# Performance work log

Hardware: AMD Instinct MI355X
Metric: run time of the kernel (lower is better)

## Reference

```python
import jax, jax.numpy as jnp
import numpy as np

NUM_HEADS = 16
THETA = 10000.0


def _rope(x, cos, sin):
    # x: [B, H, S, d_k]; cos/sin: [S, d_k//2]
    x_even = x[..., 0::2]
    x_odd = x[..., 1::2]
    out_even = x_even * cos - x_odd * sin
    out_odd = x_odd * cos + x_even * sin
    # interleave back to original even/odd layout
    return jnp.stack([out_even, out_odd], axis=-1).reshape(x.shape)


def setup_inputs() -> dict:
    key = jax.random.key(0)
    ks = jax.random.split(key, 5)
    B, S, D = 2, 2048, 1024
    std = 2.0 / (D + D)
    return {
        "x": jax.random.normal(ks[0], (B, S, D), dtype=jnp.float32),
        "w_q": jax.random.normal(ks[1], (D, D), dtype=jnp.float32) * std,
        "w_k": jax.random.normal(ks[2], (D, D), dtype=jnp.float32) * std,
        "w_v": jax.random.normal(ks[3], (D, D), dtype=jnp.float32) * std,
        "w_o": jax.random.normal(ks[4], (D, D), dtype=jnp.float32) * std,
    }


def reference(x, w_q, w_k, w_v, w_o):
    B, S, D = x.shape
    H = NUM_HEADS
    d_k = D // H

    # QKV projections: x @ W.T
    q = jnp.einsum('bsd,ed->bse', x, w_q).reshape(B, S, H, d_k).transpose(0, 2, 1, 3)
    k = jnp.einsum('bsd,ed->bse', x, w_k).reshape(B, S, H, d_k).transpose(0, 2, 1, 3)
    v = jnp.einsum('bsd,ed->bse', x, w_v).reshape(B, S, H, d_k).transpose(0, 2, 1, 3)

    # RoPE (token_positions = arange(S))
    pos = jnp.arange(S, dtype=jnp.float32)
    inv_freq = 1.0 / (THETA ** (2.0 * jnp.arange(d_k // 2, dtype=jnp.float32) / d_k))
    angles = pos[:, None] * inv_freq[None, :]  # [S, d_k//2]
    cos, sin = jnp.cos(angles), jnp.sin(angles)
    q = _rope(q, cos, sin)
    k = _rope(k, cos, sin)

    # causal attention
    scores = jnp.einsum('bhqd,bhkd->bhqk', q, k) / jnp.sqrt(jnp.float32(d_k))
    causal = jnp.tril(jnp.ones((S, S), dtype=bool))
    scores = jnp.where(causal[None, None], scores, -jnp.inf)
    attn = jax.nn.softmax(scores, axis=-1)
    out = jnp.einsum('bhqk,bhkd->bhqd', attn, v)  # [B, H, S, d_k]

    out = out.transpose(0, 2, 1, 3).reshape(B, S, D)
    return jnp.einsum('bsd,ed->bse', out, w_o)
```

## Files before the change

kernel.cpp:

```cpp
#include <hip/hip_runtime.h>

typedef unsigned short u16;
typedef unsigned int u32;
typedef short bf16x8 __attribute__((ext_vector_type(8)));
typedef float f32x4 __attribute__((ext_vector_type(4)));

#define CSC 0.18033688011112042f

__device__ __forceinline__ u16 f2bf(float f) {
    union { float f; unsigned u; } x; x.f = f;
    unsigned r = x.u + 0x7fffu + ((x.u >> 16) & 1u);
    return (u16)(r >> 16);
}
__device__ __forceinline__ float bf2f(u16 v) {
    union { unsigned u; float f; } x; x.u = ((unsigned)v) << 16;
    return x.f;
}
__device__ __forceinline__ float exp2_fast(float x) {
#if __has_builtin(__builtin_amdgcn_exp2f)
    return __builtin_amdgcn_exp2f(x);
#else
    return exp2f(x);
#endif
}
__device__ __forceinline__ void gl_lds16(const u16* g, u16* l) {
#if __has_builtin(__builtin_amdgcn_global_load_lds)
    __builtin_amdgcn_global_load_lds(
        (const __attribute__((address_space(1))) unsigned int*)g,
        (__attribute__((address_space(3))) unsigned int*)l, 16, 0, 0);
#else
    *(bf16x8*)l = *(const bf16x8*)g;
#endif
}
__device__ __forceinline__ int ileave(int x) {
    return (x < 16) ? (x << 1) : (((x - 16) << 1) | 1);
}

__global__ void cvt_all_kernel(const float* __restrict__ x, const float* __restrict__ wq,
                               const float* __restrict__ wk, const float* __restrict__ wv,
                               const float* __restrict__ wo,
                               u16* __restrict__ xb, u16* __restrict__ qkvw,
                               u16* __restrict__ ow) {
    int i = blockIdx.x * 256 + threadIdx.x;
    const float4* src;
    ushort4* dst;
    if (i < 1048576) {
        src = (const float4*)x + i;
        dst = (ushort4*)xb + i;
    } else {
        int r = i - 1048576;
        int m = r >> 18;
        int off = r & 262143;
        const float* s4 = (m == 0) ? wq : (m == 1) ? wk : (m == 2) ? wv : wo;
        u16* d = (m < 3) ? (qkvw + (size_t)m * 1048576) : ow;
        src = (const float4*)s4 + off;
        dst = (ushort4*)d + off;
    }
    float4 v = *src;
    ushort4 o;
    o.x = f2bf(v.x); o.y = f2bf(v.y); o.z = f2bf(v.z); o.w = f2bf(v.w);
    *dst = o;
}

__global__ void rope_kernel(u16* __restrict__ qb, u16* __restrict__ kb) {
    int idx = blockIdx.x * 256 + threadIdx.x;
    u16* buf;
    float scale;
    if (blockIdx.y == 0) { buf = qb; scale = CSC; } else { buf = kb; scale = 1.0f; }
    int g   = idx & 7;
    int row = idx >> 3;
    int s   = row & 2047;
    u16* p = buf + (size_t)row * 64 + g * 8;
    bf16x8 v = *(bf16x8*)p;
    bf16x8 o;
    #pragma unroll
    for (int q = 0; q < 4; ++q) {
        int i = g * 4 + q;
        float inv = exp2_fast((float)i * -0.4152410118609203f);
        float ang = (float)s * inv;
        float sn, cs;
        sincosf(ang, &sn, &cs);
        float e  = bf2f(((u16*)&v)[2 * q]);
        float od = bf2f(((u16*)&v)[2 * q + 1]);
        ((u16*)&o)[2 * q]     = f2bf((e * cs - od * sn) * scale);
        ((u16*)&o)[2 * q + 1] = f2bf((od * cs + e * sn) * scale);
    }
    *(bf16x8*)p = o;
}

__global__ __launch_bounds__(256) void gemm_qkv(const u16* __restrict__ A,
                                                const u16* __restrict__ Bw,
                                                u16* __restrict__ C, int K) {
    __shared__ __align__(16) u16 SH[8448];
    u16* As = SH;
    u16* Bs = SH + 4096;
    const int tid  = threadIdx.x;
    const int bm   = blockIdx.x * 128;
    const int bn   = blockIdx.y * 128;
    const int wave = tid >> 6, lane = tid & 63;
    const int wm   = (wave >> 1) * 64, wn = (wave & 1) * 64;
    const int l16  = lane & 15, quad = lane >> 4;
    const int mat  = bn >> 10;

    f32x4 acc[4][4];
    #pragma unroll
    for (int i = 0; i < 4; i++)
        #pragma unroll
        for (int j = 0; j < 4; j++)
            #pragma unroll
            for (int e = 0; e < 4; e++) acc[i][j][e] = 0.0f;

    const int srow = tid >> 2, scol = (tid & 3) * 8;
    const u16* gA0 = A  + (size_t)(bm + srow) * K + scol;
    const u16* gA1 = A  + (size_t)(bm + 64 + srow) * K + scol;
    const u16* gB0 = Bw + (size_t)(bn + srow) * K + scol;
    const u16* gB1 = Bw + (size_t)(bn + 64 + srow) * K + scol;
    u16* lA0 = &As[(size_t)tid * 8];
    u16* lA1 = &As[(size_t)(tid + 256) * 8];
    u16* lB0 = &Bs[(size_t)tid * 8];
    u16* lB1 = &Bs[(size_t)(tid + 256) * 8];

    for (int k0 = 0; k0 < K; k0 += 32) {
        __syncthreads();
        gl_lds16(gA0 + k0, lA0);
        gl_lds16(gA1 + k0, lA1);
        gl_lds16(gB0 + k0, lB0);
        gl_lds16(gB1 + k0, lB1);
        __syncthreads();
        bf16x8 af[4], bfr[4];
        #pragma unroll
        for (int i = 0; i < 4; i++) af[i]  = *(const bf16x8*)&As[(wm + i * 16 + l16) * 32 + quad * 8];
        #pragma unroll
        for (int j = 0; j < 4; j++) bfr[j] = *(const bf16x8*)&Bs[(wn + j * 16 + l16) * 32 + quad * 8];
        #pragma unroll
        for (int i = 0; i < 4; i++)
            #pragma unroll
            for (int j = 0; j < 4; j++)
                acc[i][j] = __builtin_amdgcn_mfma_f32_16x16x32_bf16(af[i], bfr[j], acc[i][j], 0, 0, 0);
    }

    const int b  = bm >> 11, sb = bm & 2047;
    if (mat < 2) {
        #pragma unroll
        for (int pass = 0; pass < 2; ++pass) {
            __syncthreads();
            if ((wn >> 6) == pass) {
                #pragma unroll
                for (int i = 0; i < 4; i++)
                    #pragma unroll
                    for (int j = 0; j < 4; j++)
                        #pragma unroll
                        for (int r = 0; r < 4; r++) {
                            int rl = wm + i * 16 + quad * 4 + r;
                            int cl = j * 16 + l16;
                            SH[rl * 66 + cl] = f2bf(acc[i][j][r]);
                        }
            }
            __syncthreads();
            int rl   = tid >> 1;
            int half = (tid & 1) * 32;
            int c    = (bn + pass * 64) & 1023;
            int h    = c >> 6;
            int s    = sb + rl;
            u16* dst = C + (size_t)mat * 4194304 +
                       (((size_t)(b * 16 + h) * 2048 + s) * 64) + half;
            const u16* srcp = &SH[rl * 66 + half];
            #pragma unroll
            for (int kk = 0; kk < 4; ++kk)
                *(bf16x8*)(dst + kk * 8) = *(const bf16x8*)(srcp + kk * 8);
        }
    } else {
        #pragma unroll
        for (int pass = 0; pass < 2; ++pass) {
            __syncthreads();
            if ((wn >> 6) == pass) {
                #pragma unroll
                for (int i = 0; i < 4; i++)
                    #pragma unroll
                    for (int j = 0; j < 4; j++)
                        #pragma unroll
                        for (int r = 0; r < 4; r++) {
                            int row = j * 16 + l16;
                            int ml  = wm + i * 16 + quad * 4 + r;
                            int sp  = (ml & ~31) | ileave(ml & 31);
                            SH[row * 130 + sp] = f2bf(acc[i][j][r]);
                        }
            }
            __syncthreads();
            int row = tid >> 2, seg = tid & 3;
            int cc  = (bn + pass * 64 + row) & 1023;
            int h = cc >> 6, dv = cc & 63;
            u16* dst = C + (size_t)8388608 +
                       (((size_t)(b * 16 + h) * 64 + dv) * 2048) + sb + seg * 32;
            const u16* srcp = &SH[row * 130 + seg * 32];
            #pragma unroll
            for (int kk = 0; kk < 4; ++kk)
                *(bf16x8*)(dst + kk * 8) = *(const bf16x8*)(srcp + kk * 8);
        }
    }
}

__global__ __launch_bounds__(256, 2) void gemm_out(const u16* __restrict__ A,
                                                   const u16* __restrict__ Bw,
                                                   float* __restrict__ C, int K) {
    __shared__ __align__(16) u16 As[128 * 32];
    __shared__ __align__(16) u16 Bs[64 * 32];
    const int tid  = threadIdx.x;
    const int bm   = blockIdx.x * 128;
    const int bn   = blockIdx.y * 64;
    const int wave = tid >> 6, lane = tid & 63;
    const int wm   = wave * 32;
    const int l16  = lane & 15, quad = lane >> 4;

    f32x4 acc[2][4];
    #pragma unroll
    for (int i = 0; i < 2; i++)
        #pragma unroll
        for (int j = 0; j < 4; j++)
            #pragma unroll
            for (int e = 0; e < 4; e++) acc[i][j][e] = 0.0f;

    const int srow = tid >> 2, scol = (tid & 3) * 8;
    const u16* gA0 = A  + (size_t)(bm + srow) * K + scol;
    const u16* gA1 = A  + (size_t)(bm + 64 + srow) * K + scol;
    const u16* gB0 = Bw + (size_t)(bn + srow) * K + scol;
    u16* lA0 = &As[(size_t)tid * 8];
    u16* lA1 = &As[(size_t)(tid + 256) * 8];
    u16* lB0 = &Bs[(size_t)tid * 8];

    for (int k0 = 0; k0 < K; k0 += 32) {
        __syncthreads();
        gl_lds16(gA0 + k0, lA0);
        gl_lds16(gA1 + k0, lA1);
        gl_lds16(gB0 + k0, lB0);
        __syncthreads();
        bf16x8 af[2], bfr[4];
        #pragma unroll
        for (int i = 0; i < 2; i++) af[i]  = *(const bf16x8*)&As[(wm + i * 16 + l16) * 32 + quad * 8];
        #pragma unroll
        for (int j = 0; j < 4; j++) bfr[j] = *(const bf16x8*)&Bs[(j * 16 + l16) * 32 + quad * 8];
        #pragma unroll
        for (int i = 0; i < 2; i++)
            #pragma unroll
            for (int j = 0; j < 4; j++)
                acc[i][j] = __builtin_amdgcn_mfma_f32_16x16x32_bf16(af[i], bfr[j], acc[i][j], 0, 0, 0);
    }

    #pragma unroll
    for (int i = 0; i < 2; i++)
        #pragma unroll
        for (int j = 0; j < 4; j++)
            #pragma unroll
            for (int r = 0; r < 4; r++) {
                int mr = bm + wm + i * 16 + quad * 4 + r;
                int nc = bn + j * 16 + l16;
                C[(size_t)mr * 1024 + nc] = acc[i][j][r];
            }
}

__global__ __launch_bounds__(256, 2) void attn_kernel(const u16* __restrict__ Q,
                                                      const u16* __restrict__ Kb,
                                                      const u16* __restrict__ Vt,
                                                      u16* __restrict__ Oout) {
    __shared__ __align__(16) u16 KV[2][8192];
    __shared__ __align__(16) u16 PW[4 * 1024];
    const int tid  = threadIdx.x;
    const int wave = tid >> 6, lane = tid & 63;
    const int l16  = lane & 15, quad = lane >> 4;
    const int bid  = blockIdx.x;
    const int j    = (bid >> 3) & 15;
    const int bh   = (bid & 7) * 4 + (bid >> 7);
    const int T    = 32 - j;
    const int qA0  = j * 64 + wave * 16;
    const int qB0  = (31 - j) * 64 + wave * 16;

    const u16* Qh = Q  + (size_t)bh * 2048 * 64;
    const u16* Kh = Kb + (size_t)bh * 2048 * 64;
    const u16* Vh = Vt + (size_t)bh * 64 * 2048;

    bf16x8 qAf0 = *(const bf16x8*)&Qh[(size_t)(qA0 + l16) * 64 + quad * 8];
    bf16x8 qAf1 = *(const bf16x8*)&Qh[(size_t)(qA0 + l16) * 64 + 32 + quad * 8];
    bf16x8 qBf0 = *(const bf16x8*)&Qh[(size_t)(qB0 + l16) * 64 + quad * 8];
    bf16x8 qBf1 = *(const bf16x8*)&Qh[(size_t)(qB0 + l16) * 64 + 32 + quad * 8];

    f32x4 oA[4], oB[4];
    float lsA[4], lsB[4];
    #pragma unroll
    for (int t = 0; t < 4; t++)
        #pragma unroll
        for (int e = 0; e < 4; e++) { oA[t][e] = 0.0f; oB[t][e] = 0.0f; }
    #pragma unroll
    for (int r = 0; r < 4; r++) { lsA[r] = 0.0f; lsB[r] = 0.0f; }

    const int srow = tid >> 2;
    const int scs  = (((tid & 3) ^ ((tid >> 3) & 3))) * 8;
    const u16* gK = Kh + (size_t)srow * 64 + scs;
    const u16* gV = Vh + (size_t)srow * 2048 + scs;

    const int cswz = (quad ^ ((l16 >> 1) & 3)) * 8;
    const int psw0 = ((quad ^ (l16 & 7)) << 3);
    const int psw1 = (((quad ^ (l16 & 7)) ^ 4) << 3);

    u16* pw16 = PW + wave * 1024;
    u32* pw32 = (u32*)pw16;

    auto stage = [&](int t, int buf) {
        u16* base = KV[buf];
        gl_lds16(gK + (size_t)t * 4096,      base + (size_t)tid * 8);
        gl_lds16(gK + (size_t)t * 4096 + 32, base + 2048 + (size_t)tid * 8);
        gl_lds16(gV + (size_t)t * 64,        base + 4096 + (size_t)tid * 8);
        gl_lds16(gV + (size_t)t * 64 + 32,   base + 6144 + (size_t)tid * 8);
    };

    auto side = [&](const bf16x8& q0f, const bf16x8& q1f, bf16x8* kf0, bf16x8* kf1,
                    bf16x8* vf0, bf16x8* vf1, f32x4* o, float* ls,
                    int q0, int kbase, bool diag) {
        f32x4 s[4];
        #pragma unroll
        for (int n = 0; n < 4; n++) {
            #pragma unroll
            for (int e = 0; e < 4; e++) s[n][e] = 0.0f;
            s[n] = __builtin_amdgcn_mfma_f32_16x16x32_bf16(q0f, kf0[n], s[n], 0, 0, 0);
            s[n] = __builtin_amdgcn_mfma_f32_16x16x32_bf16(q1f, kf1[n], s[n], 0, 0, 0);
        }
        float p[4][4];
        #pragma unroll
        for (int n = 0; n < 4; n++)
            #pragma unroll
            for (int r = 0; r < 4; r++) {
                float v = exp2_fast(s[n][r]);
                if (diag) {
                    int row = q0 + quad * 4 + r;
                    v = (kbase + n * 16 + l16 > row) ? 0.0f : v;
                }
                p[n][r] = v;
                ls[r] += v;
            }
        #pragma unroll
        for (int c = 0; c < 2; c++)
            #pragma unroll
            for (int r = 0; r < 4; r++) {
                int prow = quad * 4 + r;
                int pj   = (((c * 4 + (l16 >> 2)) ^ (prow & 7)) << 2) | (l16 & 3);
                pw32[prow * 32 + pj] =
                    (u32)f2bf(p[2 * c][r]) | ((u32)f2bf(p[2 * c + 1][r]) << 16);
            }
        asm volatile("s_waitcnt lgkmcnt(0)" ::: "memory");
        bf16x8 pf0 = *(const bf16x8*)&pw16[l16 * 64 + psw0];
        bf16x8 pf1 = *(const bf16x8*)&pw16[l16 * 64 + psw1];
        #pragma unroll
        for (int dn = 0; dn < 4; dn++) {
            o[dn] = __builtin_amdgcn_mfma_f32_16x16x32_bf16(pf0, vf0[dn], o[dn], 0, 0, 0);
            o[dn] = __builtin_amdgcn_mfma_f32_16x16x32_bf16(pf1, vf1[dn], o[dn], 0, 0, 0);
        }
    };

    stage(0, 0);
    for (int t = 0; t < T; ++t) {
        __syncthreads();
        if (t + 1 < T) stage(t + 1, (t + 1) & 1);
        const u16* B = KV[t & 1];
        bf16x8 kf0[4], kf1[4], vf0[4], vf1[4];
        #pragma unroll
        for (int n = 0; n < 4; n++) {
            int ri = (n * 16 + l16) * 32 + cswz;
            kf0[n] = *(const bf16x8*)&B[ri];
            kf1[n] = *(const bf16x8*)&B[2048 + ri];
            vf0[n] = *(const bf16x8*)&B[4096 + ri];
            vf1[n] = *(const bf16x8*)&B[6144 + ri];
        }
        const int kbase = t * 64;
        side(qBf0, qBf1, kf0, kf1, vf0, vf1, oB, lsB, qB0, kbase, t == T - 1);
        if (t <= j)
            side(qAf0, qAf1, kf0, kf1, vf0, vf1, oA, lsA, qA0, kbase, t == j);
    }

    #pragma unroll
    for (int off = 1; off < 16; off <<= 1)
        #pragma unroll
        for (int r = 0; r < 4; r++) {
            lsA[r] += __shfl_xor(lsA[r], off);
            lsB[r] += __shfl_xor(lsB[r], off);
        }

    const int b = bh >> 4, h = bh & 15;
    #pragma unroll
    for (int r = 0; r < 4; r++) {
        float iA = 1.0f / lsA[r];
        float iB = 1.0f / lsB[r];
        int sA = qA0 + quad * 4 + r;
        int sB = qB0 + quad * 4 + r;
        #pragma unroll
        for (int dn = 0; dn < 4; dn++) {
            int d = h * 64 + dn * 16 + l16;
            Oout[((size_t)b * 2048 + sA) * 1024 + d] = f2bf(oA[dn][r] * iA);
            Oout[((size_t)b * 2048 + sB) * 1024 + d] = f2bf(oB[dn][r] * iB);
        }
    }
}

extern "C" void kernel_launch(void* const* d_in, const int* in_sizes, int n_in,
                              void* d_out, int out_size, void* d_ws, size_t ws_size,
                              hipStream_t stream) {
    const float* x  = (const float*)d_in[0];
    const float* wq = (const float*)d_in[1];
    const float* wk = (const float*)d_in[2];
    const float* wv = (const float*)d_in[3];
    const float* wo = (const float*)d_in[4];
    float* out = (float*)d_out;

    const int M = 4096, D = 1024;
    u16* xb    = (u16*)d_ws;
    u16* qkvw  = xb   + (size_t)M * D;
    u16* ow    = qkvw + (size_t)3 * D * D;
    u16* qkv   = ow   + (size_t)D * D;
    u16* qb    = qkv;
    u16* kb    = qkv + (size_t)M * D;
    u16* vtb   = qkv + (size_t)2 * M * D;
    u16* aob   = qkv + (size_t)3 * M * D;

    cvt_all_kernel<<<8192, 256, 0, stream>>>(x, wq, wk, wv, wo, xb, qkvw, ow);

    dim3 gq(32, 24);
    gemm_qkv<<<gq, 256, 0, stream>>>(xb, qkvw, qkv, D);

    dim3 gr(2048, 2);
    rope_kernel<<<gr, 256, 0, stream>>>(qb, kb);

    attn_kernel<<<512, 256, 0, stream>>>(qb, kb, vtb, aob);

    dim3 go(32, 16);
    gemm_out<<<go, 256, 0, stream>>>(aob, ow, out, D);
}
```

Before: 195.2 us.

## Split attention KV loop across two wave groups with LDS partial-sum merge

The attention kernel now uses 512 threads per block, with two groups of four waves each handling alternating 64-key tiles of the same query rows, so per-block KV work is split in half. Each group has its own double-buffered K/V staging region in LDS. After the loop, group 1 writes its partial O accumulators and row sums to LDS and group 0 adds them before normalising and storing. This raises wave-level parallelism for the long causal rows at the cost of doubled LDS use, an extra reduction pass, and possibly lower occupancy. The merge works by plain addition because the softmax uses a fixed scale with no running max.

Result: slower. 303.9 us (+55.7%).

```diff
diff --git a/kernel.cpp b/kernel.cpp
--- a/kernel.cpp
+++ b/kernel.cpp
@@ -258,21 +258,24 @@
             }
 }
 
-__global__ __launch_bounds__(256, 2) void attn_kernel(const u16* __restrict__ Q,
+__global__ __launch_bounds__(512, 4) void attn_kernel(const u16* __restrict__ Q,
                                                       const u16* __restrict__ Kb,
                                                       const u16* __restrict__ Vt,
                                                       u16* __restrict__ Oout) {
-    __shared__ __align__(16) u16 KV[2][8192];
-    __shared__ __align__(16) u16 PW[4 * 1024];
+    __shared__ __align__(16) u16 KV[4][8192];
+    __shared__ __align__(16) u16 PW[8 * 1024];
     const int tid  = threadIdx.x;
     const int wave = tid >> 6, lane = tid & 63;
+    const int grp  = wave >> 2;
+    const int w4   = wave & 3;
+    const int tidl = tid & 255;
     const int l16  = lane & 15, quad = lane >> 4;
     const int bid  = blockIdx.x;
     const int j    = (bid >> 3) & 15;
     const int bh   = (bid & 7) * 4 + (bid >> 7);
     const int T    = 32 - j;
-    const int qA0  = j * 64 + wave * 16;
-    const int qB0  = (31 - j) * 64 + wave * 16;
+    const int qA0  = j * 64 + w4 * 16;
+    const int qB0  = (31 - j) * 64 + w4 * 16;
 
     const u16* Qh = Q  + (size_t)bh * 2048 * 64;
     const u16* Kh = Kb + (size_t)bh * 2048 * 64;
@@ -292,8 +295,8 @@
     #pragma unroll
     for (int r = 0; r < 4; r++) { lsA[r] = 0.0f; lsB[r] = 0.0f; }
 
-    const int srow = tid >> 2;
-    const int scs  = (((tid & 3) ^ ((tid >> 3) & 3))) * 8;
+    const int srow = tidl >> 2;
+    const int scs  = (((tidl & 3) ^ ((tidl >> 3) & 3))) * 8;
     const u16* gK = Kh + (size_t)srow * 64 + scs;
     const u16* gV = Vh + (size_t)srow * 2048 + scs;
 
@@ -306,10 +309,10 @@
 
     auto stage = [&](int t, int buf) {
         u16* base = KV[buf];
-        gl_lds16(gK + (size_t)t * 4096,      base + (size_t)tid * 8);
-        gl_lds16(gK + (size_t)t * 4096 + 32, base + 2048 + (size_t)tid * 8);
-        gl_lds16(gV + (size_t)t * 64,        base + 4096 + (size_t)tid * 8);
-        gl_lds16(gV + (size_t)t * 64 + 32,   base + 6144 + (size_t)tid * 8);
+        gl_lds16(gK + (size_t)t * 4096,      base + (size_t)tidl * 8);
+        gl_lds16(gK + (size_t)t * 4096 + 32, base + 2048 + (size_t)tidl * 8);
+        gl_lds16(gV + (size_t)t * 64,        base + 4096 + (size_t)tidl * 8);
+        gl_lds16(gV + (size_t)t * 64 + 32,   base + 6144 + (size_t)tidl * 8);
     };
 
     auto side = [&](const bf16x8& q0f, const bf16x8& q1f, bf16x8* kf0, bf16x8* kf1,
@@ -355,46 +358,84 @@
         }
     };
 
-    stage(0, 0);
-    for (int t = 0; t < T; ++t) {
+    stage(grp, 2 * grp);
+    const int nI = (T + 1) >> 1;
+    for (int i = 0; i < nI; ++i) {
         __syncthreads();
-        if (t + 1 < T) stage(t + 1, (t + 1) & 1);
-        const u16* B = KV[t & 1];
-        bf16x8 kf0[4], kf1[4], vf0[4], vf1[4];
-        #pragma unroll
-        for (int n = 0; n < 4; n++) {
-            int ri = (n * 16 + l16) * 32 + cswz;
-            kf0[n] = *(const bf16x8*)&B[ri];
-            kf1[n] = *(const bf16x8*)&B[2048 + ri];
-            vf0[n] = *(const bf16x8*)&B[4096 + ri];
-            vf1[n] = *(const bf16x8*)&B[6144 + ri];
-        }
-        const int kbase = t * 64;
-        side(qBf0, qBf1, kf0, kf1, vf0, vf1, oB, lsB, qB0, kbase, t == T - 1);
-        if (t <= j)
-            side(qAf0, qAf1, kf0, kf1, vf0, vf1, oA, lsA, qA0, kbase, t == j);
-    }
-
-    #pragma unroll
-    for (int off = 1; off < 16; off <<= 1)
+        const int tg = 2 * i + grp;
+        const int tn = tg + 2;
+        if (tn < T) stage(tn, 2 * grp + ((i + 1) & 1));
+        if (tg < T) {
+            const u16* B = KV[2 * grp + (i & 1)];
+            bf16x8 kf0[4], kf1[4], vf0[4], vf1[4];
+            #pragma unroll
+            for (int n = 0; n < 4; n++) {
+                int ri = (n * 16 + l16) * 32 + cswz;
+                kf0[n] = *(const bf16x8*)&B[ri];
+                kf1[n] = *(const bf16x8*)&B[2048 + ri];
+                vf0[n] = *(const bf16x8*)&B[4096 + ri];
+                vf1[n] = *(const bf16x8*)&B[6144 + ri];
+            }
+            const int kbase = tg * 64;
+            side(qBf0, qBf1, kf0, kf1, vf0, vf1, oB, lsB, qB0, kbase, tg == T - 1);
+            if (tg <= j)
+                side(qAf0, qAf1, kf0, kf1, vf0, vf1, oA, lsA, qA0, kbase, tg == j);
+        }
+    }
+
+    __syncthreads();
+    float* CB = (float*)&KV[0][0];
+    float* wb = CB + (size_t)w4 * 2560;
+    if (grp == 1) {
+        #pragma unroll
+        for (int dn = 0; dn < 4; dn++)
+            #pragma unroll
+            for (int e = 0; e < 4; e++) {
+                wb[(dn * 4 + e) * 64 + lane]        = oA[dn][e];
+                wb[1024 + (dn * 4 + e) * 64 + lane] = oB[dn][e];
+            }
         #pragma unroll
         for (int r = 0; r < 4; r++) {
-            lsA[r] += __shfl_xor(lsA[r], off);
-            lsB[r] += __shfl_xor(lsB[r], off);
-        }
-
-    const int b = bh >> 4, h = bh & 15;
-    #pragma unroll
-    for (int r = 0; r < 4; r++) {
-        float iA = 1.0f / lsA[r];
-        float iB = 1.0f / lsB[r];
-        int sA = qA0 + quad * 4 + r;
-        int sB = qB0 + quad * 4 + r;
-        #pragma unroll
-        for (int dn = 0; dn < 4; dn++) {
-            int d = h * 64 + dn * 16 + l16;
-            Oout[((size_t)b * 2048 + sA) * 1024 + d] = f2bf(oA[dn][r] * iA);
-            Oout[((size_t)b * 2048 + sB) * 1024 + d] = f2bf(oB[dn][r] * iB);
+            wb[2048 + r * 64 + lane]       = lsA[r];
+            wb[2048 + 256 + r * 64 + lane] = lsB[r];
+        }
+    }
+    __syncthreads();
+    if (grp == 0) {
+        #pragma unroll
+        for (int dn = 0; dn < 4; dn++)
+            #pragma unroll
+            for (int e = 0; e < 4; e++) {
+                oA[dn][e] += wb[(dn * 4 + e) * 64 + lane];
+                oB[dn][e] += wb[1024 + (dn * 4 + e) * 64 + lane];
+            }
+        #pragma unroll
+        for (int r = 0; r < 4; r++) {
+            lsA[r] += wb[2048 + r * 64 + lane];
+            lsB[r] += wb[2048 + 256 + r * 64 + lane];
+        }
+
+        #pragma unroll
+        for (int off = 1; off < 16; off <<= 1)
+            #pragma unroll
+            for (int r = 0; r < 4; r++) {
+                lsA[r] += __shfl_xor(lsA[r], off);
+                lsB[r] += __shfl_xor(lsB[r], off);
+            }
+
+        const int b = bh >> 4, h = bh & 15;
+        #pragma unroll
+        for (int r = 0; r < 4; r++) {
+            float iA = 1.0f / lsA[r];
+            float iB = 1.0f / lsB[r];
+            int sA = qA0 + quad * 4 + r;
+            int sB = qB0 + quad * 4 + r;
+            #pragma unroll
+            for (int dn = 0; dn < 4; dn++) {
+                int d = h * 64 + dn * 16 + l16;
+                Oout[((size_t)b * 2048 + sA) * 1024 + d] = f2bf(oA[dn][r] * iA);
+                Oout[((size_t)b * 2048 + sB) * 1024 + d] = f2bf(oB[dn][r] * iB);
+            }
         }
     }
 }
@@ -427,7 +468,7 @@
     dim3 gr(2048, 2);
     rope_kernel<<<gr, 256, 0, stream>>>(qb, kb);
 
-    attn_kernel<<<512, 256, 0, stream>>>(qb, kb, vtb, aob);
+    attn_kernel<<<512, 512, 0, stream>>>(qb, kb, vtb, aob);
 
     dim3 go(32, 16);
     gemm_out<<<go, 256, 0, stream>>>(aob, ow, out, D);
```

## Split paired causal query tiles into one tile per block, heaviest first

Applied to the files above, without the earlier changes.

Each attention block used to process a pair of query tiles (j and 31-j) that shared K/V loads. Now each block handles a single 64-row query tile, with blocks ordered so the longest causal tiles are scheduled first, and the grid doubles to 1024 blocks. Launch bounds rise to 4 blocks per CU to raise occupancy. This trades away K/V reuse across the paired tiles, so more K/V is staged from memory, in exchange for more parallelism and fewer registers per thread.

Measured after the change: 208.3 us. 6.7% more time.

```diff
diff --git a/kernel.cpp b/kernel.cpp
--- a/kernel.cpp
+++ b/kernel.cpp
@@ -258,7 +258,7 @@
             }
 }
 
-__global__ __launch_bounds__(256, 2) void attn_kernel(const u16* __restrict__ Q,
+__global__ __launch_bounds__(256, 4) void attn_kernel(const u16* __restrict__ Q,
                                                       const u16* __restrict__ Kb,
                                                       const u16* __restrict__ Vt,
                                                       u16* __restrict__ Oout) {
@@ -268,29 +268,26 @@
     const int wave = tid >> 6, lane = tid & 63;
     const int l16  = lane & 15, quad = lane >> 4;
     const int bid  = blockIdx.x;
-    const int j    = (bid >> 3) & 15;
-    const int bh   = (bid & 7) * 4 + (bid >> 7);
-    const int T    = 32 - j;
-    const int qA0  = j * 64 + wave * 16;
-    const int qB0  = (31 - j) * 64 + wave * 16;
+    const int qi   = 31 - ((bid >> 3) & 31);
+    const int bh   = (bid & 7) * 4 + (bid >> 8);
+    const int T    = qi + 1;
+    const int q0   = qi * 64 + wave * 16;
 
     const u16* Qh = Q  + (size_t)bh * 2048 * 64;
     const u16* Kh = Kb + (size_t)bh * 2048 * 64;
     const u16* Vh = Vt + (size_t)bh * 64 * 2048;
 
-    bf16x8 qAf0 = *(const bf16x8*)&Qh[(size_t)(qA0 + l16) * 64 + quad * 8];
-    bf16x8 qAf1 = *(const bf16x8*)&Qh[(size_t)(qA0 + l16) * 64 + 32 + quad * 8];
-    bf16x8 qBf0 = *(const bf16x8*)&Qh[(size_t)(qB0 + l16) * 64 + quad * 8];
-    bf16x8 qBf1 = *(const bf16x8*)&Qh[(size_t)(qB0 + l16) * 64 + 32 + quad * 8];
-
-    f32x4 oA[4], oB[4];
-    float lsA[4], lsB[4];
+    bf16x8 qf0 = *(const bf16x8*)&Qh[(size_t)(q0 + l16) * 64 + quad * 8];
+    bf16x8 qf1 = *(const bf16x8*)&Qh[(size_t)(q0 + l16) * 64 + 32 + quad * 8];
+
+    f32x4 o[4];
+    float ls[4];
     #pragma unroll
     for (int t = 0; t < 4; t++)
         #pragma unroll
-        for (int e = 0; e < 4; e++) { oA[t][e] = 0.0f; oB[t][e] = 0.0f; }
-    #pragma unroll
-    for (int r = 0; r < 4; r++) { lsA[r] = 0.0f; lsB[r] = 0.0f; }
+        for (int e = 0; e < 4; e++) o[t][e] = 0.0f;
+    #pragma unroll
+    for (int r = 0; r < 4; r++) ls[r] = 0.0f;
 
     const int srow = tid >> 2;
     const int scs  = (((tid & 3) ^ ((tid >> 3) & 3))) * 8;
@@ -312,16 +309,30 @@
         gl_lds16(gV + (size_t)t * 64 + 32,   base + 6144 + (size_t)tid * 8);
     };
 
-    auto side = [&](const bf16x8& q0f, const bf16x8& q1f, bf16x8* kf0, bf16x8* kf1,
-                    bf16x8* vf0, bf16x8* vf1, f32x4* o, float* ls,
-                    int q0, int kbase, bool diag) {
+    stage(0, 0);
+    for (int t = 0; t < T; ++t) {
+        __syncthreads();
+        if (t + 1 < T) stage(t + 1, (t + 1) & 1);
+        const u16* B = KV[t & 1];
+        bf16x8 kf0[4], kf1[4], vf0[4], vf1[4];
+        #pragma unroll
+        for (int n = 0; n < 4; n++) {
+            int ri = (n * 16 + l16) * 32 + cswz;
+            kf0[n] = *(const bf16x8*)&B[ri];
+            kf1[n] = *(const bf16x8*)&B[2048 + ri];
+            vf0[n] = *(const bf16x8*)&B[4096 + ri];
+            vf1[n] = *(const bf16x8*)&B[6144 + ri];
+        }
+        const int kbase = t * 64;
+        const bool diag = (t == qi);
+
         f32x4 s[4];
         #pragma unroll
         for (int n = 0; n < 4; n++) {
             #pragma unroll
             for (int e = 0; e < 4; e++) s[n][e] = 0.0f;
-            s[n] = __builtin_amdgcn_mfma_f32_16x16x32_bf16(q0f, kf0[n], s[n], 0, 0, 0);
-            s[n] = __builtin_amdgcn_mfma_f32_16x16x32_bf16(q1f, kf1[n], s[n], 0, 0, 0);
+            s[n] = __builtin_amdgcn_mfma_f32_16x16x32_bf16(qf0, kf0[n], s[n], 0, 0, 0);
+            s[n] = __builtin_amdgcn_mfma_f32_16x16x32_bf16(qf1, kf1[n], s[n], 0, 0, 0);
         }
         float p[4][4];
         #pragma unroll
@@ -353,48 +364,23 @@
             o[dn] = __builtin_amdgcn_mfma_f32_16x16x32_bf16(pf0, vf0[dn], o[dn], 0, 0, 0);
             o[dn] = __builtin_amdgcn_mfma_f32_16x16x32_bf16(pf1, vf1[dn], o[dn], 0, 0, 0);
         }
-    };
-
-    stage(0, 0);
-    for (int t = 0; t < T; ++t) {
-        __syncthreads();
-        if (t + 1 < T) stage(t + 1, (t + 1) & 1);
-        const u16* B = KV[t & 1];
-        bf16x8 kf0[4], kf1[4], vf0[4], vf1[4];
-        #pragma unroll
-        for (int n = 0; n < 4; n++) {
-            int ri = (n * 16 + l16) * 32 + cswz;
-            kf0[n] = *(const bf16x8*)&B[ri];
-            kf1[n] = *(const bf16x8*)&B[2048 + ri];
-            vf0[n] = *(const bf16x8*)&B[4096 + ri];
-            vf1[n] = *(const bf16x8*)&B[6144 + ri];
-        }
-        const int kbase = t * 64;
-        side(qBf0, qBf1, kf0, kf1, vf0, vf1, oB, lsB, qB0, kbase, t == T - 1);
-        if (t <= j)
-            side(qAf0, qAf1, kf0, kf1, vf0, vf1, oA, lsA, qA0, kbase, t == j);
     }
 
     #pragma unroll
     for (int off = 1; off < 16; off <<= 1)
         #pragma unroll
-        for (int r = 0; r < 4; r++) {
-            lsA[r] += __shfl_xor(lsA[r], off);
-            lsB[r] += __shfl_xor(lsB[r], off);
-        }
+        for (int r = 0; r < 4; r++)
+            ls[r] += __shfl_xor(ls[r], off);
 
     const int b = bh >> 4, h = bh & 15;
     #pragma unroll
     for (int r = 0; r < 4; r++) {
-        float iA = 1.0f / lsA[r];
-        float iB = 1.0f / lsB[r];
-        int sA = qA0 + quad * 4 + r;
-        int sB = qB0 + quad * 4 + r;
+        float inv = 1.0f / ls[r];
+        int srw = q0 + quad * 4 + r;
         #pragma unroll
         for (int dn = 0; dn < 4; dn++) {
             int d = h * 64 + dn * 16 + l16;
-            Oout[((size_t)b * 2048 + sA) * 1024 + d] = f2bf(oA[dn][r] * iA);
-            Oout[((size_t)b * 2048 + sB) * 1024 + d] = f2bf(oB[dn][r] * iB);
+            Oout[((size_t)b * 2048 + srw) * 1024 + d] = f2bf(o[dn][r] * inv);
         }
     }
 }
@@ -427,7 +413,7 @@
     dim3 gr(2048, 2);
     rope_kernel<<<gr, 256, 0, stream>>>(qb, kb);
 
-    attn_kernel<<<512, 256, 0, stream>>>(qb, kb, vtb, aob);
+    attn_kernel<<<1024, 256, 0, stream>>>(qb, kb, vtb, aob);
 
     dim3 go(32, 16);
     gemm_out<<<go, 256, 0, stream>>>(aob, ow, out, D);
```

## Load K/V fragments directly from global memory instead of LDS double buffering

Applied to the files above, without the earlier changes.

Drops the shared-memory double-buffered K/V staging and the per-tile __syncthreads, so each wave loads its MFMA K and V fragments straight from global memory into registers. The aim is to remove the barrier and LDS traffic and to free 32KB of LDS, which may allow more blocks per CU. In exchange, each of the four waves now fetches the same K/V tile separately, relying on L1/L2 to absorb the redundant loads. Global load latency is also no longer prefetched a tile ahead.

Measured after the change: 265.4 us. +36.0%, slower.

```diff
diff --git a/kernel.cpp b/kernel.cpp
--- a/kernel.cpp
+++ b/kernel.cpp
@@ -262,7 +262,6 @@
                                                       const u16* __restrict__ Kb,
                                                       const u16* __restrict__ Vt,
                                                       u16* __restrict__ Oout) {
-    __shared__ __align__(16) u16 KV[2][8192];
     __shared__ __align__(16) u16 PW[4 * 1024];
     const int tid  = threadIdx.x;
     const int wave = tid >> 6, lane = tid & 63;
@@ -292,25 +291,14 @@
     #pragma unroll
     for (int r = 0; r < 4; r++) { lsA[r] = 0.0f; lsB[r] = 0.0f; }
 
-    const int srow = tid >> 2;
-    const int scs  = (((tid & 3) ^ ((tid >> 3) & 3))) * 8;
-    const u16* gK = Kh + (size_t)srow * 64 + scs;
-    const u16* gV = Vh + (size_t)srow * 2048 + scs;
-
-    const int cswz = (quad ^ ((l16 >> 1) & 3)) * 8;
+    const u16* kB0 = Kh + (size_t)l16 * 64 + quad * 8;
+    const u16* vB0 = Vh + (size_t)l16 * 2048 + quad * 8;
+
     const int psw0 = ((quad ^ (l16 & 7)) << 3);
     const int psw1 = (((quad ^ (l16 & 7)) ^ 4) << 3);
 
     u16* pw16 = PW + wave * 1024;
     u32* pw32 = (u32*)pw16;
-
-    auto stage = [&](int t, int buf) {
-        u16* base = KV[buf];
-        gl_lds16(gK + (size_t)t * 4096,      base + (size_t)tid * 8);
-        gl_lds16(gK + (size_t)t * 4096 + 32, base + 2048 + (size_t)tid * 8);
-        gl_lds16(gV + (size_t)t * 64,        base + 4096 + (size_t)tid * 8);
-        gl_lds16(gV + (size_t)t * 64 + 32,   base + 6144 + (size_t)tid * 8);
-    };
 
     auto side = [&](const bf16x8& q0f, const bf16x8& q1f, bf16x8* kf0, bf16x8* kf1,
                     bf16x8* vf0, bf16x8* vf1, f32x4* o, float* ls,
@@ -355,21 +343,18 @@
         }
     };
 
-    stage(0, 0);
     for (int t = 0; t < T; ++t) {
-        __syncthreads();
-        if (t + 1 < T) stage(t + 1, (t + 1) & 1);
-        const u16* B = KV[t & 1];
+        const int kbase = t * 64;
         bf16x8 kf0[4], kf1[4], vf0[4], vf1[4];
         #pragma unroll
         for (int n = 0; n < 4; n++) {
-            int ri = (n * 16 + l16) * 32 + cswz;
-            kf0[n] = *(const bf16x8*)&B[ri];
-            kf1[n] = *(const bf16x8*)&B[2048 + ri];
-            vf0[n] = *(const bf16x8*)&B[4096 + ri];
-            vf1[n] = *(const bf16x8*)&B[6144 + ri];
-        }
-        const int kbase = t * 64;
+            const u16* kr = kB0 + (size_t)(kbase + n * 16) * 64;
+            const u16* vr = vB0 + (size_t)(n * 16) * 2048 + kbase;
+            kf0[n] = *(const bf16x8*)kr;
+            kf1[n] = *(const bf16x8*)(kr + 32);
+            vf0[n] = *(const bf16x8*)vr;
+            vf1[n] = *(const bf16x8*)(vr + 32);
+        }
         side(qBf0, qBf1, kf0, kf1, vf0, vf1, oB, lsB, qB0, kbase, t == T - 1);
         if (t <= j)
             side(qAf0, qAf1, kf0, kf1, vf0, vf1, oA, lsA, qA0, kbase, t == j);
```
